# Kernel optimization log

Hardware: AMD Instinct MI355X
Metric: run time of the kernel (lower is better)

## Reference

```python
import jax, jax.numpy as jnp
import numpy as np

D = 1024
H = 16
DH = D // H
SCALE = 1.0 / float(np.sqrt(DH))
EPS = 1e-5


def layer_norm(x, g, b):
    mu = jnp.mean(x, axis=-1, keepdims=True)
    var = jnp.mean((x - mu) ** 2, axis=-1, keepdims=True)
    return (x - mu) * jax.lax.rsqrt(var + EPS) * g + b


def setup_inputs() -> dict:
    key = jax.random.key(0)
    ks = jax.random.split(key, 12)
    B, N = 2, 2048
    x = jax.random.normal(ks[0], (B, N, D), dtype=jnp.float32)
    # sparse 0/1 adjacency (tree-like density) plus self loops
    adj = (jax.random.uniform(ks[1], (B, N, N)) < 0.002).astype(jnp.float32)
    adj = jnp.maximum(adj, jnp.eye(N, dtype=jnp.float32)[None])
    attn_mask = jnp.zeros((B, N, N), dtype=jnp.float32)
    s = 0.02
    params = {
        "qkv_w": jax.random.normal(ks[2], (D, 3 * D)) * s,
        "qkv_b": jnp.zeros((3 * D,), jnp.float32),
        "out_w": jax.random.normal(ks[3], (D, D)) * s,
        "out_b": jnp.zeros((D,), jnp.float32),
        "ln1_g": jnp.ones((D,), jnp.float32),
        "ln1_b": jnp.zeros((D,), jnp.float32),
        "ln2_g": jnp.ones((D,), jnp.float32),
        "ln2_b": jnp.zeros((D,), jnp.float32),
        "ff1_w": jax.random.normal(ks[4], (D, 4 * D)) * s,
        "ff1_b": jnp.zeros((4 * D,), jnp.float32),
        "ff2_w": jax.random.normal(ks[5], (4 * D, D)) * s,
        "ff2_b": jnp.zeros((D,), jnp.float32),
        "struct_bias": jnp.zeros((1,), jnp.float32) + 0.1,
    }
    return {"x": x, "adjacency": adj, "attn_mask": attn_mask, **params}


def reference(x, adjacency, attn_mask, qkv_w, qkv_b, out_w, out_b,
              ln1_g, ln1_b, ln2_g, ln2_b, ff1_w, ff1_b, ff2_w, ff2_b,
              struct_bias):
    b, n, d = x.shape
    residual = x
    h = layer_norm(x, ln1_g, ln1_b)
    qkv = (h @ qkv_w + qkv_b).reshape(b, n, 3, H, DH)
    q = jnp.transpose(qkv[:, :, 0], (0, 2, 1, 3))  # [B,H,N,Dh]
    k = jnp.transpose(qkv[:, :, 1], (0, 2, 1, 3))
    v = jnp.transpose(qkv[:, :, 2], (0, 2, 1, 3))
    scores = jnp.einsum("bhqd,bhkd->bhqk", q, k) * SCALE
    scores = scores + struct_bias[0] * adjacency[:, None] + attn_mask[:, None]
    attn = jax.nn.softmax(scores, axis=-1)  # dropout is identity at eval
    out = jnp.einsum("bhqk,bhkd->bhqd", attn, v)
    out = jnp.transpose(out, (0, 2, 1, 3)).reshape(b, n, d)
    out = out @ out_w + out_b
    x1 = residual + out
    h2 = layer_norm(x1, ln2_g, ln2_b)
    ff = jax.nn.gelu(h2 @ ff1_w + ff1_b, approximate=False) @ ff2_w + ff2_b
    return x1 + ff
```

## Files before the change

### kernel.cpp

```cpp
#include <hip/hip_runtime.h>
#include <math.h>

#define Dm 1024
#define Hh 16
#define DHh 64
#define Bb 2
#define Nn 2048
#define Rr 4096
#define SCALE_ 0.125f
#define EPS_ 1e-5f
#define SMAX_ 4.0f

typedef unsigned short u16;
typedef __attribute__((ext_vector_type(8))) short short8;
typedef __attribute__((ext_vector_type(4))) float f32x4;

__device__ __forceinline__ u16 f2bf(float f) {
  union { float f; unsigned u; } v; v.f = f;
  unsigned r = v.u + 0x7fffu + ((v.u >> 16) & 1u);
  return (u16)(r >> 16);
}
__device__ __forceinline__ float bf2f(u16 h) {
  union { unsigned u; float f; } v; v.u = ((unsigned)h) << 16;
  return v.f;
}

__device__ __forceinline__ void g2l16(const u16* g, const u16* l) {
  __builtin_amdgcn_global_load_lds(
      (const __attribute__((address_space(1))) void*)g,
      (__attribute__((address_space(3))) void*)l, 16, 0, 0);
}

__global__ void transpose_to_bf16(const float* __restrict__ W, u16* __restrict__ WT,
                                  int K, int N) {
  __shared__ float tile[32][33];
  int n0 = blockIdx.x * 32, k0 = blockIdx.y * 32;
  int tx = threadIdx.x, ty = threadIdx.y;
#pragma unroll
  for (int i = 0; i < 4; i++)
    tile[ty + 8 * i][tx] = W[(size_t)(k0 + ty + 8 * i) * N + n0 + tx];
  __syncthreads();
#pragma unroll
  for (int i = 0; i < 4; i++)
    WT[(size_t)(n0 + ty + 8 * i) * K + k0 + tx] = f2bf(tile[tx][ty + 8 * i]);
}

__global__ void bias_precompute(const float* __restrict__ adj, const float* __restrict__ mask,
                                const float* __restrict__ sbp, u16* __restrict__ bias16) {
  const float sb = sbp[0];
  size_t i = ((size_t)blockIdx.x * 256 + threadIdx.x) * 8;
  float4 a0 = *(const float4*)(adj + i);
  float4 a1 = *(const float4*)(adj + i + 4);
  float4 m0 = *(const float4*)(mask + i);
  float4 m1 = *(const float4*)(mask + i + 4);
  ushort4 o0, o1;
  o0.x = f2bf(sb * a0.x + m0.x); o0.y = f2bf(sb * a0.y + m0.y);
  o0.z = f2bf(sb * a0.z + m0.z); o0.w = f2bf(sb * a0.w + m0.w);
  o1.x = f2bf(sb * a1.x + m1.x); o1.y = f2bf(sb * a1.y + m1.y);
  o1.z = f2bf(sb * a1.z + m1.z); o1.w = f2bf(sb * a1.w + m1.w);
  *(ushort4*)(bias16 + i) = o0;
  *(ushort4*)(bias16 + i + 4) = o1;
}

__global__ void ln_kernel(const float* __restrict__ x, const float* __restrict__ g,
                          const float* __restrict__ be, u16* __restrict__ out) {
  int row = blockIdx.x;
  int t = threadIdx.x;
  float4 v = ((const float4*)(x + (size_t)row * Dm))[t];
  float s = v.x + v.y + v.z + v.w;
  float s2 = v.x * v.x + v.y * v.y + v.z * v.z + v.w * v.w;
#pragma unroll
  for (int o = 32; o > 0; o >>= 1) { s += __shfl_down(s, o); s2 += __shfl_down(s2, o); }
  __shared__ float sm[8];
  int w = t >> 6;
  if ((t & 63) == 0) { sm[w] = s; sm[4 + w] = s2; }
  __syncthreads();
  if (t == 0) {
    float a = sm[0] + sm[1] + sm[2] + sm[3];
    float a2 = sm[4] + sm[5] + sm[6] + sm[7];
    float mu = a * (1.f / Dm);
    sm[0] = mu;
    sm[1] = rsqrtf(a2 * (1.f / Dm) - mu * mu + EPS_);
  }
  __syncthreads();
  float mu = sm[0], rstd = sm[1];
  float4 gv = ((const float4*)g)[t];
  float4 bv = ((const float4*)be)[t];
  ushort4 o4;
  o4.x = f2bf((v.x - mu) * rstd * gv.x + bv.x);
  o4.y = f2bf((v.y - mu) * rstd * gv.y + bv.y);
  o4.z = f2bf((v.z - mu) * rstd * gv.z + bv.z);
  o4.w = f2bf((v.w - mu) * rstd * gv.w + bv.w);
  ((ushort4*)(out + (size_t)row * Dm))[t] = o4;
}

template <int MODE, int IT>
__global__ __launch_bounds__(256) void gemm_bt(
    const u16* __restrict__ A, const u16* __restrict__ BT,
    const float* __restrict__ bias, const float* __restrict__ res,
    void* __restrict__ Cout, u16* __restrict__ qb,
    u16* __restrict__ kb, u16* __restrict__ vb, int Ndim, int Kdim) {
  constexpr int TM = IT * 32;
  constexpr int AI = TM / 16;
  __shared__ u16 As[TM * 32];
  __shared__ u16 Bs[128 * 32];
  const int t = threadIdx.x;
  const int wave = t >> 6, lane = t & 63;
  const int wm = wave >> 1, wn = wave & 1;
  const int lr = lane & 15, lq = lane >> 4;
  const int m0 = blockIdx.y * TM, n0 = blockIdx.x * 128;
  const int srow = lane >> 2, scol = (lane & 3) * 8;
  f32x4 acc[IT][4];
#pragma unroll
  for (int i = 0; i < IT; i++)
#pragma unroll
    for (int j = 0; j < 4; j++) acc[i][j] = (f32x4){0.f, 0.f, 0.f, 0.f};

  for (int kt = 0; kt < Kdim; kt += 32) {
    __syncthreads();
    for (int s = wave; s < AI + 8; s += 4) {
      if (s < AI)
        g2l16(A + (size_t)(m0 + s * 16 + srow) * Kdim + kt + scol, &As[(s * 16) * 32]);
      else
        g2l16(BT + (size_t)(n0 + (s - AI) * 16 + srow) * Kdim + kt + scol,
              &Bs[((s - AI) * 16) * 32]);
    }
    __syncthreads();
    short8 af[IT], bf[4];
#pragma unroll
    for (int i = 0; i < IT; i++)
      af[i] = *(const short8*)&As[(wm * (IT * 16) + i * 16 + lr) * 32 + lq * 8];
#pragma unroll
    for (int j = 0; j < 4; j++)
      bf[j] = *(const short8*)&Bs[(wn * 64 + j * 16 + lr) * 32 + lq * 8];
#pragma unroll
    for (int i = 0; i < IT; i++)
#pragma unroll
      for (int j = 0; j < 4; j++)
        acc[i][j] = __builtin_amdgcn_mfma_f32_16x16x32_bf16(af[i], bf[j], acc[i][j], 0, 0, 0);
  }

#pragma unroll
  for (int i = 0; i < IT; i++) {
#pragma unroll
    for (int j = 0; j < 4; j++) {
#pragma unroll
      for (int r = 0; r < 4; r++) {
        int row = m0 + wm * (IT * 16) + i * 16 + lq * 4 + r;
        int col = n0 + wn * 64 + j * 16 + lr;
        float val = acc[i][j][r] + bias[col];
        if (MODE == 0) {
          int s = col >> 10, rem = col & 1023;
          int hh = rem >> 6, dh = rem & 63;
          int bi = row >> 11, ni = row & 2047;
          if (s == 2) {
            vb[(((size_t)bi * Hh + hh) * DHh + dh) * Nn + ni] = f2bf(val);
          } else {
            u16* dst = (s == 0) ? qb : kb;
            dst[(((size_t)bi * Hh + hh) * Nn + ni) * DHh + dh] = f2bf(val);
          }
        } else if (MODE == 1 || MODE == 3) {
          size_t o = (size_t)row * Ndim + col;
          ((float*)Cout)[o] = val + res[o];
        } else {
          size_t o = (size_t)row * Ndim + col;
          float gv = 0.5f * val * (1.f + erff(val * 0.70710678118f));
          ((u16*)Cout)[o] = f2bf(gv);
        }
      }
    }
  }
}

__global__ __launch_bounds__(256) void attn_kernel(
    const u16* __restrict__ q, const u16* __restrict__ k, const u16* __restrict__ vT,
    const u16* __restrict__ bias16, u16* __restrict__ out) {
  const int qt = blockIdx.x, hh = blockIdx.y, b = blockIdx.z;
  const int t = threadIdx.x, wave = t >> 6, lane = t & 63;
  const int lr = lane & 15, lq = lane >> 4;
  const size_t head_off = (((size_t)b * Hh + hh) * Nn) * DHh;
  const u16* Q = q + head_off;
  const u16* K = k + head_off;
  const u16* Vt = vT + head_off;
  const int q0 = qt * 128;

  __shared__ u16 Ks[64 * 72];
  __shared__ u16 VsT[64 * 72];
  __shared__ u16 Ps[4][32 * 72];

  short8 qf[2][2];
#pragma unroll
  for (int qs = 0; qs < 2; qs++) {
    const u16* Qr = Q + (size_t)(q0 + wave * 32 + qs * 16 + lr) * DHh;
    qf[qs][0] = *(const short8*)(Qr + lq * 8);
    qf[qs][1] = *(const short8*)(Qr + 32 + lq * 8);
  }
  f32x4 o_acc[2][4];
  float l_acc[2][4];
#pragma unroll
  for (int qs = 0; qs < 2; qs++) {
#pragma unroll
    for (int j = 0; j < 4; j++) o_acc[qs][j] = (f32x4){0.f, 0.f, 0.f, 0.f};
#pragma unroll
    for (int r = 0; r < 4; r++) l_acc[qs][r] = 0.f;
  }

  const int srow = t >> 2;
  const int sc0 = (t & 3) * 16;
  const int ssw = ((srow >> 2) & 3) << 4;
  const int wc0 = sc0 ^ ssw, wc1 = (sc0 + 8) ^ ssw;
  const u16* Kst = K + (size_t)srow * DHh + sc0;
  const u16* Vst = Vt + (size_t)srow * Nn + sc0;
  const int rsw = ((lr >> 2) & 3) << 4;

  const u16* bp = bias16 + ((size_t)b * Nn + q0 + wave * 32 + lq * 4) * Nn + lr;

  f32x4 kr0 = *(const f32x4*)(Kst);
  f32x4 kr1 = *(const f32x4*)(Kst + 8);
  f32x4 vr0 = *(const f32x4*)(Vst);
  f32x4 vr1 = *(const f32x4*)(Vst + 8);
  unsigned short bw[2][4][4];
#pragma unroll
  for (int qs = 0; qs < 2; qs++)
#pragma unroll
    for (int ns = 0; ns < 4; ns++)
#pragma unroll
      for (int r = 0; r < 4; r++)
        bw[qs][ns][r] = bp[(size_t)(qs * 16 + r) * Nn + ns * 16];

  for (int kt = 0; kt < Nn; kt += 64) {
    __syncthreads();
    *(f32x4*)&Ks[srow * 72 + wc0] = kr0;
    *(f32x4*)&Ks[srow * 72 + wc1] = kr1;
    *(f32x4*)&VsT[srow * 72 + wc0] = vr0;
    *(f32x4*)&VsT[srow * 72 + wc1] = vr1;
    __syncthreads();
    if (kt + 64 < Nn) {
      kr0 = *(const f32x4*)(Kst + (size_t)(kt + 64) * DHh);
      kr1 = *(const f32x4*)(Kst + (size_t)(kt + 64) * DHh + 8);
      vr0 = *(const f32x4*)(Vst + kt + 64);
      vr1 = *(const f32x4*)(Vst + kt + 64 + 8);
    }
    short8 kf[4][2];
#pragma unroll
    for (int ns = 0; ns < 4; ns++) {
      int row = ns * 16 + lr;
      kf[ns][0] = *(const short8*)&Ks[row * 72 + ((lq * 8) ^ rsw)];
      kf[ns][1] = *(const short8*)&Ks[row * 72 + ((32 + lq * 8) ^ rsw)];
    }
    f32x4 s0[4], s1[4];
#pragma unroll
    for (int ns = 0; ns < 4; ns++) {
      s0[ns] = (f32x4){0.f, 0.f, 0.f, 0.f};
      s1[ns] = (f32x4){0.f, 0.f, 0.f, 0.f};
      s0[ns] = __builtin_amdgcn_mfma_f32_16x16x32_bf16(qf[0][0], kf[ns][0], s0[ns], 0, 0, 0);
      s0[ns] = __builtin_amdgcn_mfma_f32_16x16x32_bf16(qf[0][1], kf[ns][1], s0[ns], 0, 0, 0);
      s1[ns] = __builtin_amdgcn_mfma_f32_16x16x32_bf16(qf[1][0], kf[ns][0], s1[ns], 0, 0, 0);
      s1[ns] = __builtin_amdgcn_mfma_f32_16x16x32_bf16(qf[1][1], kf[ns][1], s1[ns], 0, 0, 0);
    }
    float p0[4][4], p1[4][4];
#pragma unroll
    for (int ns = 0; ns < 4; ns++)
#pragma unroll
      for (int r = 0; r < 4; r++) {
        p0[ns][r] = __expf(s0[ns][r] * SCALE_ + bf2f(bw[0][ns][r]) - SMAX_);
        p1[ns][r] = __expf(s1[ns][r] * SCALE_ + bf2f(bw[1][ns][r]) - SMAX_);
        l_acc[0][r] += p0[ns][r];
        l_acc[1][r] += p1[ns][r];
      }
    if (kt + 64 < Nn) {
#pragma unroll
      for (int qs = 0; qs < 2; qs++)
#pragma unroll
        for (int ns = 0; ns < 4; ns++)
#pragma unroll
          for (int r = 0; r < 4; r++)
            bw[qs][ns][r] = bp[(size_t)(qs * 16 + r) * Nn + kt + 64 + ns * 16];
    }
#pragma unroll
    for (int ns = 0; ns < 4; ns++) {
      int csw = ((ns ^ lq) * 16) + lr;
#pragma unroll
      for (int r = 0; r < 4; r++) {
        Ps[wave][(lq * 4 + r) * 72 + csw] = f2bf(p0[ns][r]);
        Ps[wave][(16 + lq * 4 + r) * 72 + csw] = f2bf(p1[ns][r]);
      }
    }
    short8 pf[2][2];
#pragma unroll
    for (int qs = 0; qs < 2; qs++) {
      pf[qs][0] = *(const short8*)&Ps[wave][(qs * 16 + lr) * 72 + ((lq * 8) ^ rsw)];
      pf[qs][1] = *(const short8*)&Ps[wave][(qs * 16 + lr) * 72 + ((32 + lq * 8) ^ rsw)];
    }
#pragma unroll
    for (int j = 0; j < 4; j++) {
      int row = j * 16 + lr;
      short8 vf0 = *(const short8*)&VsT[row * 72 + ((lq * 8) ^ rsw)];
      short8 vf1 = *(const short8*)&VsT[row * 72 + ((32 + lq * 8) ^ rsw)];
      o_acc[0][j] = __builtin_amdgcn_mfma_f32_16x16x32_bf16(pf[0][0], vf0, o_acc[0][j], 0, 0, 0);
      o_acc[0][j] = __builtin_amdgcn_mfma_f32_16x16x32_bf16(pf[0][1], vf1, o_acc[0][j], 0, 0, 0);
      o_acc[1][j] = __builtin_amdgcn_mfma_f32_16x16x32_bf16(pf[1][0], vf0, o_acc[1][j], 0, 0, 0);
      o_acc[1][j] = __builtin_amdgcn_mfma_f32_16x16x32_bf16(pf[1][1], vf1, o_acc[1][j], 0, 0, 0);
    }
  }
#pragma unroll
  for (int qs = 0; qs < 2; qs++)
#pragma unroll
    for (int r = 0; r < 4; r++) {
#pragma unroll
      for (int o = 1; o < 16; o <<= 1) l_acc[qs][r] += __shfl_xor(l_acc[qs][r], o);
      float inv = 1.0f / l_acc[qs][r];
      int qrow = q0 + wave * 32 + qs * 16 + lq * 4 + r;
#pragma unroll
      for (int j = 0; j < 4; j++) {
        out[((size_t)(b * Nn + qrow)) * Dm + hh * DHh + j * 16 + lr] =
            f2bf(o_acc[qs][j][r] * inv);
      }
    }
}

extern "C" void kernel_launch(void* const* d_in, const int* in_sizes, int n_in,
                              void* d_out, int out_size, void* d_ws, size_t ws_size,
                              hipStream_t stream) {
  const float* x     = (const float*)d_in[0];
  const float* adj   = (const float*)d_in[1];
  const float* amask = (const float*)d_in[2];
  const float* qkv_w = (const float*)d_in[3];
  const float* qkv_b = (const float*)d_in[4];
  const float* out_w = (const float*)d_in[5];
  const float* out_b = (const float*)d_in[6];
  const float* ln1_g = (const float*)d_in[7];
  const float* ln1_b = (const float*)d_in[8];
  const float* ln2_g = (const float*)d_in[9];
  const float* ln2_b = (const float*)d_in[10];
  const float* ff1_w = (const float*)d_in[11];
  const float* ff1_b = (const float*)d_in[12];
  const float* ff2_w = (const float*)d_in[13];
  const float* ff2_b = (const float*)d_in[14];
  const float* sbias = (const float*)d_in[15];

  char* w = (char*)d_ws;
  const size_t MB = 1024 * 1024;
  u16* h      = (u16*)(w);
  u16* qb     = (u16*)(w + 8 * MB);
  u16* kb     = (u16*)(w + 16 * MB);
  u16* vb     = (u16*)(w + 24 * MB);
  u16* ao     = (u16*)(w + 32 * MB);
  float* x1   = (float*)(w + 40 * MB);
  u16* qkvT   = (u16*)(w + 56 * MB);
  u16* outT   = (u16*)(w + 62 * MB);
  u16* ff1T   = (u16*)(w + 64 * MB);
  u16* ff2T   = (u16*)(w + 72 * MB);
  u16* bias16 = (u16*)(w + 80 * MB);
  u16* ffo    = qb;

  transpose_to_bf16<<<dim3(3072 / 32, 1024 / 32), dim3(32, 8), 0, stream>>>(qkv_w, qkvT, 1024, 3072);
  transpose_to_bf16<<<dim3(1024 / 32, 1024 / 32), dim3(32, 8), 0, stream>>>(out_w, outT, 1024, 1024);
  transpose_to_bf16<<<dim3(4096 / 32, 1024 / 32), dim3(32, 8), 0, stream>>>(ff1_w, ff1T, 1024, 4096);
  transpose_to_bf16<<<dim3(1024 / 32, 4096 / 32), dim3(32, 8), 0, stream>>>(ff2_w, ff2T, 4096, 1024);

  bias_precompute<<<dim3((Bb * Nn * Nn) / (8 * 256)), dim3(256), 0, stream>>>(adj, amask, sbias, bias16);

  ln_kernel<<<dim3(Rr), dim3(256), 0, stream>>>(x, ln1_g, ln1_b, h);

  gemm_bt<0, 4><<<dim3(3072 / 128, 4096 / 128), dim3(256), 0, stream>>>(
      h, qkvT, qkv_b, nullptr, nullptr, qb, kb, vb, 3072, 1024);

  attn_kernel<<<dim3(Nn / 128, Hh, Bb), dim3(256), 0, stream>>>(qb, kb, vb, bias16, ao);

  gemm_bt<1, 2><<<dim3(1024 / 128, 4096 / 64), dim3(256), 0, stream>>>(
      ao, outT, out_b, x, (void*)x1, nullptr, nullptr, nullptr, 1024, 1024);

  ln_kernel<<<dim3(Rr), dim3(256), 0, stream>>>(x1, ln2_g, ln2_b, h);

  gemm_bt<2, 4><<<dim3(4096 / 128, 4096 / 128), dim3(256), 0, stream>>>(
      h, ff1T, ff1_b, nullptr, (void*)ffo, nullptr, nullptr, nullptr, 4096, 1024);

  gemm_bt<3, 2><<<dim3(1024 / 128, 4096 / 64), dim3(256), 0, stream>>>(
      ffo, ff2T, ff2_b, x1, d_out, nullptr, nullptr, nullptr, 1024, 4096);
}
```

Measured before the change: 517.5 us.

## Retile GEMMs and attention, store x1 in bf16, use exp2 softmax

GEMM tiles become configurable in M and N. The out-proj and FF2 GEMMs move to 64x64 tiles, and all GEMM blocks are remapped M-major through a flattened block index for L2 reuse of the weights. Attention now uses 64-query blocks with one 16-row slice per wave, giving more blocks and lower register pressure, and ordered so each head's K/V is shared across neighbouring blocks. Softmax switches to exp2 with folded constants and truncating bf16 conversion of P. The residual x1 is stored in bf16 to halve its traffic, which loses precision in the residual path and the second layer norm.

Result: no change. 514.5 us (-0.6%).

```diff
diff --git a/kernel.cpp b/kernel.cpp
--- a/kernel.cpp
+++ b/kernel.cpp
@@ -10,6 +10,7 @@
 #define SCALE_ 0.125f
 #define EPS_ 1e-5f
 #define SMAX_ 4.0f
+#define LOG2E_ 1.4426950408889634f
 
 typedef unsigned short u16;
 typedef __attribute__((ext_vector_type(8))) short short8;
@@ -19,6 +20,10 @@
   union { float f; unsigned u; } v; v.f = f;
   unsigned r = v.u + 0x7fffu + ((v.u >> 16) & 1u);
   return (u16)(r >> 16);
+}
+__device__ __forceinline__ u16 f2bf_t(float f) {
+  union { float f; unsigned u; } v; v.f = f;
+  return (u16)(v.u >> 16);
 }
 __device__ __forceinline__ float bf2f(u16 h) {
   union { unsigned u; float f; } v; v.u = ((unsigned)h) << 16;
@@ -62,11 +67,18 @@
   *(ushort4*)(bias16 + i + 4) = o1;
 }
 
-__global__ void ln_kernel(const float* __restrict__ x, const float* __restrict__ g,
+template <int BI>
+__global__ void ln_kernel(const void* __restrict__ xin, const float* __restrict__ g,
                           const float* __restrict__ be, u16* __restrict__ out) {
   int row = blockIdx.x;
   int t = threadIdx.x;
-  float4 v = ((const float4*)(x + (size_t)row * Dm))[t];
+  float4 v;
+  if (BI) {
+    ushort4 uv = ((const ushort4*)((const u16*)xin + (size_t)row * Dm))[t];
+    v.x = bf2f(uv.x); v.y = bf2f(uv.y); v.z = bf2f(uv.z); v.w = bf2f(uv.w);
+  } else {
+    v = ((const float4*)((const float*)xin + (size_t)row * Dm))[t];
+  }
   float s = v.x + v.y + v.z + v.w;
   float s2 = v.x * v.x + v.y * v.y + v.z * v.z + v.w * v.w;
 #pragma unroll
@@ -94,60 +106,62 @@
   ((ushort4*)(out + (size_t)row * Dm))[t] = o4;
 }
 
-template <int MODE, int IT>
+template <int MODE, int MI, int NI>
 __global__ __launch_bounds__(256) void gemm_bt(
     const u16* __restrict__ A, const u16* __restrict__ BT,
-    const float* __restrict__ bias, const float* __restrict__ res,
+    const float* __restrict__ bias, const void* __restrict__ res,
     void* __restrict__ Cout, u16* __restrict__ qb,
     u16* __restrict__ kb, u16* __restrict__ vb, int Ndim, int Kdim) {
-  constexpr int TM = IT * 32;
-  constexpr int AI = TM / 16;
+  constexpr int TM = MI * 32, TN = NI * 32;
+  constexpr int NS = (TM + TN) / 16;
   __shared__ u16 As[TM * 32];
-  __shared__ u16 Bs[128 * 32];
+  __shared__ u16 Bs[TN * 32];
   const int t = threadIdx.x;
   const int wave = t >> 6, lane = t & 63;
   const int wm = wave >> 1, wn = wave & 1;
   const int lr = lane & 15, lq = lane >> 4;
-  const int m0 = blockIdx.y * TM, n0 = blockIdx.x * 128;
-  const int srow = lane >> 2, scol = (lane & 3) * 8;
-  f32x4 acc[IT][4];
-#pragma unroll
-  for (int i = 0; i < IT; i++)
-#pragma unroll
-    for (int j = 0; j < 4; j++) acc[i][j] = (f32x4){0.f, 0.f, 0.f, 0.f};
+  const int flat = blockIdx.x + gridDim.x * blockIdx.y;
+  constexpr int nMb = 4096 / TM;
+  const int m0 = (flat % nMb) * TM, n0 = (flat / nMb) * TN;
+  f32x4 acc[MI][NI];
+#pragma unroll
+  for (int i = 0; i < MI; i++)
+#pragma unroll
+    for (int j = 0; j < NI; j++) acc[i][j] = (f32x4){0.f, 0.f, 0.f, 0.f};
 
   for (int kt = 0; kt < Kdim; kt += 32) {
     __syncthreads();
-    for (int s = wave; s < AI + 8; s += 4) {
-      if (s < AI)
-        g2l16(A + (size_t)(m0 + s * 16 + srow) * Kdim + kt + scol, &As[(s * 16) * 32]);
+    for (int s = wave; s < NS; s += 4) {
+      if (s < TM / 16)
+        g2l16(A + (size_t)(m0 + s * 16 + (lane >> 2)) * Kdim + kt + (lane & 3) * 8,
+              &As[(s * 16) * 32]);
       else
-        g2l16(BT + (size_t)(n0 + (s - AI) * 16 + srow) * Kdim + kt + scol,
-              &Bs[((s - AI) * 16) * 32]);
+        g2l16(BT + (size_t)(n0 + (s - TM / 16) * 16 + (lane >> 2)) * Kdim + kt + (lane & 3) * 8,
+              &Bs[((s - TM / 16) * 16) * 32]);
     }
     __syncthreads();
-    short8 af[IT], bf[4];
-#pragma unroll
-    for (int i = 0; i < IT; i++)
-      af[i] = *(const short8*)&As[(wm * (IT * 16) + i * 16 + lr) * 32 + lq * 8];
-#pragma unroll
-    for (int j = 0; j < 4; j++)
-      bf[j] = *(const short8*)&Bs[(wn * 64 + j * 16 + lr) * 32 + lq * 8];
-#pragma unroll
-    for (int i = 0; i < IT; i++)
-#pragma unroll
-      for (int j = 0; j < 4; j++)
+    short8 af[MI], bf[NI];
+#pragma unroll
+    for (int i = 0; i < MI; i++)
+      af[i] = *(const short8*)&As[(wm * (MI * 16) + i * 16 + lr) * 32 + lq * 8];
+#pragma unroll
+    for (int j = 0; j < NI; j++)
+      bf[j] = *(const short8*)&Bs[(wn * (NI * 16) + j * 16 + lr) * 32 + lq * 8];
+#pragma unroll
+    for (int i = 0; i < MI; i++)
+#pragma unroll
+      for (int j = 0; j < NI; j++)
         acc[i][j] = __builtin_amdgcn_mfma_f32_16x16x32_bf16(af[i], bf[j], acc[i][j], 0, 0, 0);
   }
 
 #pragma unroll
-  for (int i = 0; i < IT; i++) {
-#pragma unroll
-    for (int j = 0; j < 4; j++) {
+  for (int i = 0; i < MI; i++) {
+#pragma unroll
+    for (int j = 0; j < NI; j++) {
 #pragma unroll
       for (int r = 0; r < 4; r++) {
-        int row = m0 + wm * (IT * 16) + i * 16 + lq * 4 + r;
-        int col = n0 + wn * 64 + j * 16 + lr;
+        int row = m0 + wm * (MI * 16) + i * 16 + lq * 4 + r;
+        int col = n0 + wn * (NI * 16) + j * 16 + lr;
         float val = acc[i][j][r] + bias[col];
         if (MODE == 0) {
           int s = col >> 10, rem = col & 1023;
@@ -159,9 +173,12 @@
             u16* dst = (s == 0) ? qb : kb;
             dst[(((size_t)bi * Hh + hh) * Nn + ni) * DHh + dh] = f2bf(val);
           }
-        } else if (MODE == 1 || MODE == 3) {
+        } else if (MODE == 1) {
           size_t o = (size_t)row * Ndim + col;
-          ((float*)Cout)[o] = val + res[o];
+          ((u16*)Cout)[o] = f2bf(val + ((const float*)res)[o]);
+        } else if (MODE == 3) {
+          size_t o = (size_t)row * Ndim + col;
+          ((float*)Cout)[o] = val + bf2f(((const u16*)res)[o]);
         } else {
           size_t o = (size_t)row * Ndim + col;
           float gv = 0.5f * val * (1.f + erff(val * 0.70710678118f));
@@ -175,35 +192,33 @@
 __global__ __launch_bounds__(256) void attn_kernel(
     const u16* __restrict__ q, const u16* __restrict__ k, const u16* __restrict__ vT,
     const u16* __restrict__ bias16, u16* __restrict__ out) {
-  const int qt = blockIdx.x, hh = blockIdx.y, b = blockIdx.z;
+  const int flat = blockIdx.x + gridDim.x * blockIdx.y;
+  const int hb = flat & 31, qi = flat >> 5;
+  const int hh = hb & 15, b = hb >> 4;
+  const int q0 = qi * 64;
   const int t = threadIdx.x, wave = t >> 6, lane = t & 63;
   const int lr = lane & 15, lq = lane >> 4;
   const size_t head_off = (((size_t)b * Hh + hh) * Nn) * DHh;
   const u16* Q = q + head_off;
   const u16* K = k + head_off;
   const u16* Vt = vT + head_off;
-  const int q0 = qt * 128;
 
   __shared__ u16 Ks[64 * 72];
   __shared__ u16 VsT[64 * 72];
-  __shared__ u16 Ps[4][32 * 72];
-
-  short8 qf[2][2];
-#pragma unroll
-  for (int qs = 0; qs < 2; qs++) {
-    const u16* Qr = Q + (size_t)(q0 + wave * 32 + qs * 16 + lr) * DHh;
-    qf[qs][0] = *(const short8*)(Qr + lq * 8);
-    qf[qs][1] = *(const short8*)(Qr + 32 + lq * 8);
-  }
-  f32x4 o_acc[2][4];
-  float l_acc[2][4];
-#pragma unroll
-  for (int qs = 0; qs < 2; qs++) {
-#pragma unroll
-    for (int j = 0; j < 4; j++) o_acc[qs][j] = (f32x4){0.f, 0.f, 0.f, 0.f};
-#pragma unroll
-    for (int r = 0; r < 4; r++) l_acc[qs][r] = 0.f;
-  }
+  __shared__ u16 Ps[4][16 * 72];
+
+  short8 qf[2];
+  {
+    const u16* Qr = Q + (size_t)(q0 + wave * 16 + lr) * DHh;
+    qf[0] = *(const short8*)(Qr + lq * 8);
+    qf[1] = *(const short8*)(Qr + 32 + lq * 8);
+  }
+  f32x4 o_acc[4];
+  float l_acc[4];
+#pragma unroll
+  for (int j = 0; j < 4; j++) o_acc[j] = (f32x4){0.f, 0.f, 0.f, 0.f};
+#pragma unroll
+  for (int r = 0; r < 4; r++) l_acc[r] = 0.f;
 
   const int srow = t >> 2;
   const int sc0 = (t & 3) * 16;
@@ -213,20 +228,20 @@
   const u16* Vst = Vt + (size_t)srow * Nn + sc0;
   const int rsw = ((lr >> 2) & 3) << 4;
 
-  const u16* bp = bias16 + ((size_t)b * Nn + q0 + wave * 32 + lq * 4) * Nn + lr;
+  const u16* bp = bias16 + ((size_t)b * Nn + q0 + wave * 16 + lq * 4) * Nn + lr;
 
   f32x4 kr0 = *(const f32x4*)(Kst);
   f32x4 kr1 = *(const f32x4*)(Kst + 8);
   f32x4 vr0 = *(const f32x4*)(Vst);
   f32x4 vr1 = *(const f32x4*)(Vst + 8);
-  unsigned short bw[2][4][4];
-#pragma unroll
-  for (int qs = 0; qs < 2; qs++)
-#pragma unroll
-    for (int ns = 0; ns < 4; ns++)
-#pragma unroll
-      for (int r = 0; r < 4; r++)
-        bw[qs][ns][r] = bp[(size_t)(qs * 16 + r) * Nn + ns * 16];
+  unsigned short bw[4][4];
+#pragma unroll
+  for (int ns = 0; ns < 4; ns++)
+#pragma unroll
+    for (int r = 0; r < 4; r++) bw[ns][r] = bp[(size_t)r * Nn + ns * 16];
+
+  const float C1 = SCALE_ * LOG2E_;
+  const float C3 = -SMAX_ * LOG2E_;
 
   for (int kt = 0; kt < Nn; kt += 64) {
     __syncthreads();
@@ -241,82 +256,62 @@
       vr0 = *(const f32x4*)(Vst + kt + 64);
       vr1 = *(const f32x4*)(Vst + kt + 64 + 8);
     }
-    short8 kf[4][2];
+    f32x4 sacc[4];
 #pragma unroll
     for (int ns = 0; ns < 4; ns++) {
       int row = ns * 16 + lr;
-      kf[ns][0] = *(const short8*)&Ks[row * 72 + ((lq * 8) ^ rsw)];
-      kf[ns][1] = *(const short8*)&Ks[row * 72 + ((32 + lq * 8) ^ rsw)];
-    }
-    f32x4 s0[4], s1[4];
-#pragma unroll
-    for (int ns = 0; ns < 4; ns++) {
-      s0[ns] = (f32x4){0.f, 0.f, 0.f, 0.f};
-      s1[ns] = (f32x4){0.f, 0.f, 0.f, 0.f};
-      s0[ns] = __builtin_amdgcn_mfma_f32_16x16x32_bf16(qf[0][0], kf[ns][0], s0[ns], 0, 0, 0);
-      s0[ns] = __builtin_amdgcn_mfma_f32_16x16x32_bf16(qf[0][1], kf[ns][1], s0[ns], 0, 0, 0);
-      s1[ns] = __builtin_amdgcn_mfma_f32_16x16x32_bf16(qf[1][0], kf[ns][0], s1[ns], 0, 0, 0);
-      s1[ns] = __builtin_amdgcn_mfma_f32_16x16x32_bf16(qf[1][1], kf[ns][1], s1[ns], 0, 0, 0);
-    }
-    float p0[4][4], p1[4][4];
+      short8 kf0 = *(const short8*)&Ks[row * 72 + ((lq * 8) ^ rsw)];
+      short8 kf1 = *(const short8*)&Ks[row * 72 + ((32 + lq * 8) ^ rsw)];
+      sacc[ns] = (f32x4){0.f, 0.f, 0.f, 0.f};
+      sacc[ns] = __builtin_amdgcn_mfma_f32_16x16x32_bf16(qf[0], kf0, sacc[ns], 0, 0, 0);
+      sacc[ns] = __builtin_amdgcn_mfma_f32_16x16x32_bf16(qf[1], kf1, sacc[ns], 0, 0, 0);
+    }
+    float p[4][4];
 #pragma unroll
     for (int ns = 0; ns < 4; ns++)
 #pragma unroll
       for (int r = 0; r < 4; r++) {
-        p0[ns][r] = __expf(s0[ns][r] * SCALE_ + bf2f(bw[0][ns][r]) - SMAX_);
-        p1[ns][r] = __expf(s1[ns][r] * SCALE_ + bf2f(bw[1][ns][r]) - SMAX_);
-        l_acc[0][r] += p0[ns][r];
-        l_acc[1][r] += p1[ns][r];
+        float tt = fmaf(sacc[ns][r], C1, fmaf(bf2f(bw[ns][r]), LOG2E_, C3));
+        p[ns][r] = exp2f(tt);
+        l_acc[r] += p[ns][r];
       }
     if (kt + 64 < Nn) {
 #pragma unroll
-      for (int qs = 0; qs < 2; qs++)
-#pragma unroll
-        for (int ns = 0; ns < 4; ns++)
-#pragma unroll
-          for (int r = 0; r < 4; r++)
-            bw[qs][ns][r] = bp[(size_t)(qs * 16 + r) * Nn + kt + 64 + ns * 16];
+      for (int ns = 0; ns < 4; ns++)
+#pragma unroll
+        for (int r = 0; r < 4; r++)
+          bw[ns][r] = bp[(size_t)r * Nn + kt + 64 + ns * 16];
     }
 #pragma unroll
     for (int ns = 0; ns < 4; ns++) {
-      int csw = ((ns ^ lq) * 16) + lr;
-#pragma unroll
-      for (int r = 0; r < 4; r++) {
-        Ps[wave][(lq * 4 + r) * 72 + csw] = f2bf(p0[ns][r]);
-        Ps[wave][(16 + lq * 4 + r) * 72 + csw] = f2bf(p1[ns][r]);
-      }
-    }
-    short8 pf[2][2];
-#pragma unroll
-    for (int qs = 0; qs < 2; qs++) {
-      pf[qs][0] = *(const short8*)&Ps[wave][(qs * 16 + lr) * 72 + ((lq * 8) ^ rsw)];
-      pf[qs][1] = *(const short8*)&Ps[wave][(qs * 16 + lr) * 72 + ((32 + lq * 8) ^ rsw)];
-    }
+      int csw = ((ns ^ lq) << 4) + lr;
+#pragma unroll
+      for (int r = 0; r < 4; r++)
+        Ps[wave][(lq * 4 + r) * 72 + csw] = f2bf_t(p[ns][r]);
+    }
+    short8 pf0 = *(const short8*)&Ps[wave][lr * 72 + ((lq * 8) ^ rsw)];
+    short8 pf1 = *(const short8*)&Ps[wave][lr * 72 + ((32 + lq * 8) ^ rsw)];
 #pragma unroll
     for (int j = 0; j < 4; j++) {
       int row = j * 16 + lr;
       short8 vf0 = *(const short8*)&VsT[row * 72 + ((lq * 8) ^ rsw)];
       short8 vf1 = *(const short8*)&VsT[row * 72 + ((32 + lq * 8) ^ rsw)];
-      o_acc[0][j] = __builtin_amdgcn_mfma_f32_16x16x32_bf16(pf[0][0], vf0, o_acc[0][j], 0, 0, 0);
-      o_acc[0][j] = __builtin_amdgcn_mfma_f32_16x16x32_bf16(pf[0][1], vf1, o_acc[0][j], 0, 0, 0);
-      o_acc[1][j] = __builtin_amdgcn_mfma_f32_16x16x32_bf16(pf[1][0], vf0, o_acc[1][j], 0, 0, 0);
-      o_acc[1][j] = __builtin_amdgcn_mfma_f32_16x16x32_bf16(pf[1][1], vf1, o_acc[1][j], 0, 0, 0);
-    }
-  }
-#pragma unroll
-  for (int qs = 0; qs < 2; qs++)
-#pragma unroll
-    for (int r = 0; r < 4; r++) {
-#pragma unroll
-      for (int o = 1; o < 16; o <<= 1) l_acc[qs][r] += __shfl_xor(l_acc[qs][r], o);
-      float inv = 1.0f / l_acc[qs][r];
-      int qrow = q0 + wave * 32 + qs * 16 + lq * 4 + r;
-#pragma unroll
-      for (int j = 0; j < 4; j++) {
-        out[((size_t)(b * Nn + qrow)) * Dm + hh * DHh + j * 16 + lr] =
-            f2bf(o_acc[qs][j][r] * inv);
-      }
-    }
+      o_acc[j] = __builtin_amdgcn_mfma_f32_16x16x32_bf16(pf0, vf0, o_acc[j], 0, 0, 0);
+      o_acc[j] = __builtin_amdgcn_mfma_f32_16x16x32_bf16(pf1, vf1, o_acc[j], 0, 0, 0);
+    }
+  }
+#pragma unroll
+  for (int r = 0; r < 4; r++) {
+#pragma unroll
+    for (int o = 1; o < 16; o <<= 1) l_acc[r] += __shfl_xor(l_acc[r], o);
+    float inv = 1.0f / l_acc[r];
+    int qrow = q0 + wave * 16 + lq * 4 + r;
+#pragma unroll
+    for (int j = 0; j < 4; j++) {
+      out[((size_t)(b * Nn + qrow)) * Dm + hh * DHh + j * 16 + lr] =
+          f2bf(o_acc[j][r] * inv);
+    }
+  }
 }
 
 extern "C" void kernel_launch(void* const* d_in, const int* in_sizes, int n_in,
@@ -346,7 +341,7 @@
   u16* kb     = (u16*)(w + 16 * MB);
   u16* vb     = (u16*)(w + 24 * MB);
   u16* ao     = (u16*)(w + 32 * MB);
-  float* x1   = (float*)(w + 40 * MB);
+  u16* x1     = (u16*)(w + 40 * MB);
   u16* qkvT   = (u16*)(w + 56 * MB);
   u16* outT   = (u16*)(w + 62 * MB);
   u16* ff1T   = (u16*)(w + 64 * MB);
@@ -361,21 +356,21 @@
 
   bias_precompute<<<dim3((Bb * Nn * Nn) / (8 * 256)), dim3(256), 0, stream>>>(adj, amask, sbias, bias16);
 
-  ln_kernel<<<dim3(Rr), dim3(256), 0, stream>>>(x, ln1_g, ln1_b, h);
-
-  gemm_bt<0, 4><<<dim3(3072 / 128, 4096 / 128), dim3(256), 0, stream>>>(
+  ln_kernel<0><<<dim3(Rr), dim3(256), 0, stream>>>(x, ln1_g, ln1_b, h);
+
+  gemm_bt<0, 4, 4><<<dim3(3072 / 128, 4096 / 128), dim3(256), 0, stream>>>(
       h, qkvT, qkv_b, nullptr, nullptr, qb, kb, vb, 3072, 1024);
 
-  attn_kernel<<<dim3(Nn / 128, Hh, Bb), dim3(256), 0, stream>>>(qb, kb, vb, bias16, ao);
-
-  gemm_bt<1, 2><<<dim3(1024 / 128, 4096 / 64), dim3(256), 0, stream>>>(
+  attn_kernel<<<dim3(32, 32), dim3(256), 0, stream>>>(qb, kb, vb, bias16, ao);
+
+  gemm_bt<1, 2, 2><<<dim3(1024 / 64, 4096 / 64), dim3(256), 0, stream>>>(
       ao, outT, out_b, x, (void*)x1, nullptr, nullptr, nullptr, 1024, 1024);
 
-  ln_kernel<<<dim3(Rr), dim3(256), 0, stream>>>(x1, ln2_g, ln2_b, h);
-
-  gemm_bt<2, 4><<<dim3(4096 / 128, 4096 / 128), dim3(256), 0, stream>>>(
+  ln_kernel<1><<<dim3(Rr), dim3(256), 0, stream>>>(x1, ln2_g, ln2_b, h);
+
+  gemm_bt<2, 4, 4><<<dim3(4096 / 128, 4096 / 128), dim3(256), 0, stream>>>(
       h, ff1T, ff1_b, nullptr, (void*)ffo, nullptr, nullptr, nullptr, 4096, 1024);
 
-  gemm_bt<3, 2><<<dim3(1024 / 128, 4096 / 64), dim3(256), 0, stream>>>(
+  gemm_bt<3, 2, 2><<<dim3(1024 / 64, 4096 / 64), dim3(256), 0, stream>>>(
       ffo, ff2T, ff2_b, x1, d_out, nullptr, nullptr, nullptr, 1024, 4096);
 }
```

## Double-buffer GEMM loads, remap tiles per XCD, store x1 in bf16, tune attention exp

Applied to the files above, without the earlier changes.

The GEMM now double-buffers its LDS tiles so the next K-slice's global-to-LDS loads are issued before the current slice's MFMAs, which removes one barrier per iteration. It also remaps block indices so each XCD works on a contiguous range of M tiles, and the output-projection and FF2 GEMMs use smaller 64x64 tiles. The residual x1 is stored as bf16 instead of fp32, with LN2 and FF2 adapted to read it, which cuts traffic but loses residual precision. In attention, the exp is folded into a single exp2 with FMAs, P is converted to bf16 by truncation, and the head/batch grid dimensions are flattened.

Measured after the change: 495.2 us. 1.05x faster.

```diff
diff --git a/kernel.cpp b/kernel.cpp
--- a/kernel.cpp
+++ b/kernel.cpp
@@ -10,6 +10,7 @@
 #define SCALE_ 0.125f
 #define EPS_ 1e-5f
 #define SMAX_ 4.0f
+#define LOG2E_ 1.4426950408889634f
 
 typedef unsigned short u16;
 typedef __attribute__((ext_vector_type(8))) short short8;
@@ -19,6 +20,10 @@
   union { float f; unsigned u; } v; v.f = f;
   unsigned r = v.u + 0x7fffu + ((v.u >> 16) & 1u);
   return (u16)(r >> 16);
+}
+__device__ __forceinline__ u16 f2bf_t(float f) {
+  union { float f; unsigned u; } v; v.f = f;
+  return (u16)(v.u >> 16);
 }
 __device__ __forceinline__ float bf2f(u16 h) {
   union { unsigned u; float f; } v; v.u = ((unsigned)h) << 16;
@@ -62,11 +67,18 @@
   *(ushort4*)(bias16 + i + 4) = o1;
 }
 
-__global__ void ln_kernel(const float* __restrict__ x, const float* __restrict__ g,
+template <int BI>
+__global__ void ln_kernel(const void* __restrict__ xin, const float* __restrict__ g,
                           const float* __restrict__ be, u16* __restrict__ out) {
   int row = blockIdx.x;
   int t = threadIdx.x;
-  float4 v = ((const float4*)(x + (size_t)row * Dm))[t];
+  float4 v;
+  if (BI) {
+    ushort4 uv = ((const ushort4*)((const u16*)xin + (size_t)row * Dm))[t];
+    v.x = bf2f(uv.x); v.y = bf2f(uv.y); v.z = bf2f(uv.z); v.w = bf2f(uv.w);
+  } else {
+    v = ((const float4*)((const float*)xin + (size_t)row * Dm))[t];
+  }
   float s = v.x + v.y + v.z + v.w;
   float s2 = v.x * v.x + v.y * v.y + v.z * v.z + v.w * v.w;
 #pragma unroll
@@ -94,60 +106,73 @@
   ((ushort4*)(out + (size_t)row * Dm))[t] = o4;
 }
 
-template <int MODE, int IT>
+template <int MODE, int MI, int NI>
 __global__ __launch_bounds__(256) void gemm_bt(
     const u16* __restrict__ A, const u16* __restrict__ BT,
-    const float* __restrict__ bias, const float* __restrict__ res,
+    const float* __restrict__ bias, const void* __restrict__ res,
     void* __restrict__ Cout, u16* __restrict__ qb,
     u16* __restrict__ kb, u16* __restrict__ vb, int Ndim, int Kdim) {
-  constexpr int TM = IT * 32;
-  constexpr int AI = TM / 16;
-  __shared__ u16 As[TM * 32];
-  __shared__ u16 Bs[128 * 32];
+  constexpr int TM = MI * 32, TN = NI * 32;
+  constexpr int NS = (TM + TN) / 16;
+  __shared__ u16 As[2][TM * 32];
+  __shared__ u16 Bs[2][TN * 32];
   const int t = threadIdx.x;
   const int wave = t >> 6, lane = t & 63;
   const int wm = wave >> 1, wn = wave & 1;
   const int lr = lane & 15, lq = lane >> 4;
-  const int m0 = blockIdx.y * TM, n0 = blockIdx.x * 128;
-  const int srow = lane >> 2, scol = (lane & 3) * 8;
-  f32x4 acc[IT][4];
-#pragma unroll
-  for (int i = 0; i < IT; i++)
-#pragma unroll
-    for (int j = 0; j < 4; j++) acc[i][j] = (f32x4){0.f, 0.f, 0.f, 0.f};
-
+  const int flat = blockIdx.x + gridDim.x * blockIdx.y;
+  constexpr int nMb = 4096 / TM;
+  constexpr int mpx = nMb / 8;
+  const int xcd = flat & 7;
+  const int p = flat >> 3;
+  const int m0 = (xcd * mpx + (p % mpx)) * TM;
+  const int n0 = (p / mpx) * TN;
+
+  auto stage = [&](int kt, int bsel) {
+    for (int s = wave; s < NS; s += 4) {
+      if (s < TM / 16)
+        g2l16(A + (size_t)(m0 + s * 16 + (lane >> 2)) * Kdim + kt + (lane & 3) * 8,
+              &As[bsel][(s * 16) * 32]);
+      else
+        g2l16(BT + (size_t)(n0 + (s - TM / 16) * 16 + (lane >> 2)) * Kdim + kt + (lane & 3) * 8,
+              &Bs[bsel][((s - TM / 16) * 16) * 32]);
+    }
+  };
+
+  f32x4 acc[MI][NI];
+#pragma unroll
+  for (int i = 0; i < MI; i++)
+#pragma unroll
+    for (int j = 0; j < NI; j++) acc[i][j] = (f32x4){0.f, 0.f, 0.f, 0.f};
+
+  stage(0, 0);
+  int cur = 0;
   for (int kt = 0; kt < Kdim; kt += 32) {
     __syncthreads();
-    for (int s = wave; s < AI + 8; s += 4) {
-      if (s < AI)
-        g2l16(A + (size_t)(m0 + s * 16 + srow) * Kdim + kt + scol, &As[(s * 16) * 32]);
-      else
-        g2l16(BT + (size_t)(n0 + (s - AI) * 16 + srow) * Kdim + kt + scol,
-              &Bs[((s - AI) * 16) * 32]);
-    }
-    __syncthreads();
-    short8 af[IT], bf[4];
-#pragma unroll
-    for (int i = 0; i < IT; i++)
-      af[i] = *(const short8*)&As[(wm * (IT * 16) + i * 16 + lr) * 32 + lq * 8];
-#pragma unroll
-    for (int j = 0; j < 4; j++)
-      bf[j] = *(const short8*)&Bs[(wn * 64 + j * 16 + lr) * 32 + lq * 8];
-#pragma unroll
-    for (int i = 0; i < IT; i++)
-#pragma unroll
-      for (int j = 0; j < 4; j++)
+    if (kt + 32 < Kdim) stage(kt + 32, cur ^ 1);
+    short8 af[MI], bf[NI];
+#pragma unroll
+    for (int i = 0; i < MI; i++)
+      af[i] = *(const short8*)&As[cur][(wm * (MI * 16) + i * 16 + lr) * 32 + lq * 8];
+#pragma unroll
+    for (int j = 0; j < NI; j++)
+      bf[j] = *(const short8*)&Bs[cur][(wn * (NI * 16) + j * 16 + lr) * 32 + lq * 8];
+#pragma unroll
+    for (int i = 0; i < MI; i++)
+#pragma unroll
+      for (int j = 0; j < NI; j++)
         acc[i][j] = __builtin_amdgcn_mfma_f32_16x16x32_bf16(af[i], bf[j], acc[i][j], 0, 0, 0);
-  }
-
-#pragma unroll
-  for (int i = 0; i < IT; i++) {
-#pragma unroll
-    for (int j = 0; j < 4; j++) {
+    cur ^= 1;
+  }
+
+#pragma unroll
+  for (int i = 0; i < MI; i++) {
+#pragma unroll
+    for (int j = 0; j < NI; j++) {
 #pragma unroll
       for (int r = 0; r < 4; r++) {
-        int row = m0 + wm * (IT * 16) + i * 16 + lq * 4 + r;
-        int col = n0 + wn * 64 + j * 16 + lr;
+        int row = m0 + wm * (MI * 16) + i * 16 + lq * 4 + r;
+        int col = n0 + wn * (NI * 16) + j * 16 + lr;
         float val = acc[i][j][r] + bias[col];
         if (MODE == 0) {
           int s = col >> 10, rem = col & 1023;
@@ -159,9 +184,12 @@
             u16* dst = (s == 0) ? qb : kb;
             dst[(((size_t)bi * Hh + hh) * Nn + ni) * DHh + dh] = f2bf(val);
           }
-        } else if (MODE == 1 || MODE == 3) {
+        } else if (MODE == 1) {
           size_t o = (size_t)row * Ndim + col;
-          ((float*)Cout)[o] = val + res[o];
+          ((u16*)Cout)[o] = f2bf(val + ((const float*)res)[o]);
+        } else if (MODE == 3) {
+          size_t o = (size_t)row * Ndim + col;
+          ((float*)Cout)[o] = val + bf2f(((const u16*)res)[o]);
         } else {
           size_t o = (size_t)row * Ndim + col;
           float gv = 0.5f * val * (1.f + erff(val * 0.70710678118f));
@@ -175,7 +203,8 @@
 __global__ __launch_bounds__(256) void attn_kernel(
     const u16* __restrict__ q, const u16* __restrict__ k, const u16* __restrict__ vT,
     const u16* __restrict__ bias16, u16* __restrict__ out) {
-  const int qt = blockIdx.x, hh = blockIdx.y, b = blockIdx.z;
+  const int qt = blockIdx.x, hb = blockIdx.y;
+  const int hh = hb & 15, b = hb >> 4;
   const int t = threadIdx.x, wave = t >> 6, lane = t & 63;
   const int lr = lane & 15, lq = lane >> 4;
   const size_t head_off = (((size_t)b * Hh + hh) * Nn) * DHh;
@@ -227,6 +256,9 @@
 #pragma unroll
       for (int r = 0; r < 4; r++)
         bw[qs][ns][r] = bp[(size_t)(qs * 16 + r) * Nn + ns * 16];
+
+  const float C1 = SCALE_ * LOG2E_;
+  const float C3 = -SMAX_ * LOG2E_;
 
   for (int kt = 0; kt < Nn; kt += 64) {
     __syncthreads();
@@ -263,8 +295,8 @@
     for (int ns = 0; ns < 4; ns++)
 #pragma unroll
       for (int r = 0; r < 4; r++) {
-        p0[ns][r] = __expf(s0[ns][r] * SCALE_ + bf2f(bw[0][ns][r]) - SMAX_);
-        p1[ns][r] = __expf(s1[ns][r] * SCALE_ + bf2f(bw[1][ns][r]) - SMAX_);
+        p0[ns][r] = exp2f(fmaf(s0[ns][r], C1, fmaf(bf2f(bw[0][ns][r]), LOG2E_, C3)));
+        p1[ns][r] = exp2f(fmaf(s1[ns][r], C1, fmaf(bf2f(bw[1][ns][r]), LOG2E_, C3)));
         l_acc[0][r] += p0[ns][r];
         l_acc[1][r] += p1[ns][r];
       }
@@ -279,11 +311,11 @@
     }
 #pragma unroll
     for (int ns = 0; ns < 4; ns++) {
-      int csw = ((ns ^ lq) * 16) + lr;
+      int csw = ((ns ^ lq) << 4) + lr;
 #pragma unroll
       for (int r = 0; r < 4; r++) {
-        Ps[wave][(lq * 4 + r) * 72 + csw] = f2bf(p0[ns][r]);
-        Ps[wave][(16 + lq * 4 + r) * 72 + csw] = f2bf(p1[ns][r]);
+        Ps[wave][(lq * 4 + r) * 72 + csw] = f2bf_t(p0[ns][r]);
+        Ps[wave][(16 + lq * 4 + r) * 72 + csw] = f2bf_t(p1[ns][r]);
       }
     }
     short8 pf[2][2];
@@ -346,7 +378,7 @@
   u16* kb     = (u16*)(w + 16 * MB);
   u16* vb     = (u16*)(w + 24 * MB);
   u16* ao     = (u16*)(w + 32 * MB);
-  float* x1   = (float*)(w + 40 * MB);
+  u16* x1     = (u16*)(w + 40 * MB);
   u16* qkvT   = (u16*)(w + 56 * MB);
   u16* outT   = (u16*)(w + 62 * MB);
   u16* ff1T   = (u16*)(w + 64 * MB);
@@ -361,21 +393,21 @@
 
   bias_precompute<<<dim3((Bb * Nn * Nn) / (8 * 256)), dim3(256), 0, stream>>>(adj, amask, sbias, bias16);
 
-  ln_kernel<<<dim3(Rr), dim3(256), 0, stream>>>(x, ln1_g, ln1_b, h);
-
-  gemm_bt<0, 4><<<dim3(3072 / 128, 4096 / 128), dim3(256), 0, stream>>>(
+  ln_kernel<0><<<dim3(Rr), dim3(256), 0, stream>>>(x, ln1_g, ln1_b, h);
+
+  gemm_bt<0, 4, 4><<<dim3(3072 / 128, 4096 / 128), dim3(256), 0, stream>>>(
       h, qkvT, qkv_b, nullptr, nullptr, qb, kb, vb, 3072, 1024);
 
-  attn_kernel<<<dim3(Nn / 128, Hh, Bb), dim3(256), 0, stream>>>(qb, kb, vb, bias16, ao);
-
-  gemm_bt<1, 2><<<dim3(1024 / 128, 4096 / 64), dim3(256), 0, stream>>>(
+  attn_kernel<<<dim3(16, 32), dim3(256), 0, stream>>>(qb, kb, vb, bias16, ao);
+
+  gemm_bt<1, 2, 2><<<dim3(1024 / 64, 4096 / 64), dim3(256), 0, stream>>>(
       ao, outT, out_b, x, (void*)x1, nullptr, nullptr, nullptr, 1024, 1024);
 
-  ln_kernel<<<dim3(Rr), dim3(256), 0, stream>>>(x1, ln2_g, ln2_b, h);
-
-  gemm_bt<2, 4><<<dim3(4096 / 128, 4096 / 128), dim3(256), 0, stream>>>(
+  ln_kernel<1><<<dim3(Rr), dim3(256), 0, stream>>>(x1, ln2_g, ln2_b, h);
+
+  gemm_bt<2, 4, 4><<<dim3(4096 / 128, 4096 / 128), dim3(256), 0, stream>>>(
       h, ff1T, ff1_b, nullptr, (void*)ffo, nullptr, nullptr, nullptr, 4096, 1024);
 
-  gemm_bt<3, 2><<<dim3(1024 / 128, 4096 / 64), dim3(256), 0, stream>>>(
+  gemm_bt<3, 2, 2><<<dim3(1024 / 64, 4096 / 64), dim3(256), 0, stream>>>(
       ffo, ff2T, ff2_b, x1, d_out, nullptr, nullptr, nullptr, 1024, 4096);
 }
```
